# Kernel tuning notes

Measured on AMD Instinct MI355X. Metric: run time of the kernel, lower is better.

Reference implementation:

```python
import jax, jax.numpy as jnp
import numpy as np

EPSILON = 1e-4
MAX_ITER = 10


def setup_inputs() -> dict:
    key = jax.random.key(0)
    k1, k2, k3 = jax.random.split(key, 3)
    B, N, M = 64, 1024, 1024
    s = jax.random.uniform(k1, (B, N, M), dtype=jnp.float32)
    nrows = jax.random.randint(k2, (B,), 0, N, dtype=jnp.int32)
    ncols = jax.random.randint(k3, (B,), 0, M, dtype=jnp.int32)
    return {"s": s, "nrows": nrows, "ncols": ncols}


def reference(s, nrows, ncols):
    # s: [B, N, M]; nrows/ncols: [B] valid row/col counts per sample.
    B, N, M = s.shape
    row_mask = jnp.arange(N, dtype=nrows.dtype)[None, :] < nrows[:, None]  # [B, N]
    col_mask = jnp.arange(M, dtype=ncols.dtype)[None, :] < ncols[:, None]  # [B, M]
    mask = row_mask[:, :, None] & col_mask[:, None, :]  # [B, N, M]

    s = s + EPSILON
    for i in range(MAX_ITER):
        # i even -> column normalization (sum over dim 1); i odd -> row normalization (sum over dim 2)
        axis = 2 if i % 2 == 1 else 1
        ssum = jnp.sum(s, axis=axis, keepdims=True)
        tmp = jnp.where(mask, 1.0 / ssum, jnp.zeros((), dtype=s.dtype))
        s = s * tmp
    return s
```

## Files before the change

kernel.cpp:

```cpp
#include <hip/hip_runtime.h>

#define EPS 1e-4f

constexpr int Bn = 64;
constexpr int Nn = 1024;
constexpr int Mn = 1024;
constexpr int NSPLIT = 16;
constexpr int CHUNK  = Nn / NSPLIT;
constexpr int SLOTS  = 2 * NSPLIT;

__device__ __forceinline__ unsigned pk2(float a, float b) {
    unsigned ua = __float_as_uint(a); ua = (ua + 0x7fffu + ((ua >> 16) & 1u)) >> 16;
    unsigned ub = __float_as_uint(b); ub = (ub + 0x7fffu + ((ub >> 16) & 1u)) >> 16;
    return ua | (ub << 16);
}
__device__ __forceinline__ float lo16(unsigned v) { return __uint_as_float(v << 16); }
__device__ __forceinline__ float hi16(unsigned v) { return __uint_as_float(v & 0xffff0000u); }

__global__ __launch_bounds__(256) void fuse0_kernel(
        const float* __restrict__ s, unsigned short* __restrict__ sc,
        float* __restrict__ p) {
    const int b = blockIdx.x, sp = blockIdx.y;
    const int t = threadIdx.x, half = t >> 7, tc = t & 127;
    float acc[8];
    #pragma unroll
    for (int k = 0; k < 8; ++k) acc[k] = 0.f;
    for (int j = 0; j < CHUNK; j += 2) {
        const int n = sp * CHUNK + j + half;
        const size_t roff = ((size_t)b * Nn + n) * Mn;
        const float4* src = reinterpret_cast<const float4*>(s + roff) + 2 * tc;
        float4 v0 = src[0], v1 = src[1];
        v0.x += EPS; v0.y += EPS; v0.z += EPS; v0.w += EPS;
        v1.x += EPS; v1.y += EPS; v1.z += EPS; v1.w += EPS;
        acc[0] += v0.x; acc[1] += v0.y; acc[2] += v0.z; acc[3] += v0.w;
        acc[4] += v1.x; acc[5] += v1.y; acc[6] += v1.z; acc[7] += v1.w;
        uint4 w = { pk2(v0.x, v0.y), pk2(v0.z, v0.w),
                    pk2(v1.x, v1.y), pk2(v1.z, v1.w) };
        reinterpret_cast<uint4*>(sc + roff)[tc] = w;
    }
    float* pp = p + ((size_t)(b * SLOTS + sp * 2 + half)) * Mn + tc * 8;
    float4 o0 = {acc[0], acc[1], acc[2], acc[3]};
    float4 o1 = {acc[4], acc[5], acc[6], acc[7]};
    *reinterpret_cast<float4*>(pp)     = o0;
    *reinterpret_cast<float4*>(pp + 4) = o1;
}

__global__ __launch_bounds__(256) void colred_kernel(
        const unsigned short* __restrict__ sc, const float* __restrict__ r,
        float* __restrict__ p) {
    const int b = blockIdx.x, sp = blockIdx.y;
    const int t = threadIdx.x, half = t >> 7, tc = t & 127;
    const float* rb = r + (size_t)b * Nn;
    float acc[8];
    #pragma unroll
    for (int k = 0; k < 8; ++k) acc[k] = 0.f;
    #pragma unroll 4
    for (int j = 0; j < CHUNK; j += 2) {
        const int n = sp * CHUNK + j + half;
        uint4 a = reinterpret_cast<const uint4*>(sc + ((size_t)b * Nn + n) * Mn)[tc];
        const float rn = rb[n];
        acc[0] += lo16(a.x) * rn; acc[1] += hi16(a.x) * rn;
        acc[2] += lo16(a.y) * rn; acc[3] += hi16(a.y) * rn;
        acc[4] += lo16(a.z) * rn; acc[5] += hi16(a.z) * rn;
        acc[6] += lo16(a.w) * rn; acc[7] += hi16(a.w) * rn;
    }
    float* pp = p + ((size_t)(b * SLOTS + sp * 2 + half)) * Mn + tc * 8;
    float4 o0 = {acc[0], acc[1], acc[2], acc[3]};
    float4 o1 = {acc[4], acc[5], acc[6], acc[7]};
    *reinterpret_cast<float4*>(pp)     = o0;
    *reinterpret_cast<float4*>(pp + 4) = o1;
}

__global__ __launch_bounds__(256) void col_final_kernel(
        const float* __restrict__ p, const int* __restrict__ ncols,
        float* __restrict__ c) {
    const int b = blockIdx.x;
    const int m0 = threadIdx.x << 2;
    float sx = 0.f, sy = 0.f, sz = 0.f, sw = 0.f;
    #pragma unroll
    for (int k = 0; k < SLOTS; ++k) {
        float4 v = *reinterpret_cast<const float4*>(
            p + ((size_t)(b * SLOTS + k)) * Mn + m0);
        sx += v.x; sy += v.y; sz += v.z; sw += v.w;
    }
    const int nc = ncols[b];
    float4 o;
    o.x = (m0 + 0 < nc && sx > 0.f) ? 1.f / sx : 0.f;
    o.y = (m0 + 1 < nc && sy > 0.f) ? 1.f / sy : 0.f;
    o.z = (m0 + 2 < nc && sz > 0.f) ? 1.f / sz : 0.f;
    o.w = (m0 + 3 < nc && sw > 0.f) ? 1.f / sw : 0.f;
    *reinterpret_cast<float4*>(c + (size_t)b * Mn + m0) = o;
}

__global__ __launch_bounds__(256) void rowred_kernel(
        const unsigned short* __restrict__ sc, const float* __restrict__ c,
        const int* __restrict__ nrows, float* __restrict__ r) {
    const int b = blockIdx.x;
    const int t = threadIdx.x, w = t >> 6, l = t & 63;
    const int n0 = blockIdx.y * 32 + w * 8;
    const float4* cb = reinterpret_cast<const float4*>(c + (size_t)b * Mn);
    const float4 c0 = cb[2 * l], c1 = cb[2 * l + 1];
    const float4 c2 = cb[128 + 2 * l], c3 = cb[128 + 2 * l + 1];
    const int nr = nrows[b];
    for (int j = 0; j < 8; ++j) {
        const int n = n0 + j;
        const uint4* row = reinterpret_cast<const uint4*>(sc + ((size_t)b * Nn + n) * Mn);
        uint4 a = row[l], d = row[64 + l];
        float part =
            lo16(a.x) * c0.x + hi16(a.x) * c0.y + lo16(a.y) * c0.z + hi16(a.y) * c0.w +
            lo16(a.z) * c1.x + hi16(a.z) * c1.y + lo16(a.w) * c1.z + hi16(a.w) * c1.w +
            lo16(d.x) * c2.x + hi16(d.x) * c2.y + lo16(d.y) * c2.z + hi16(d.y) * c2.w +
            lo16(d.z) * c3.x + hi16(d.z) * c3.y + lo16(d.w) * c3.z + hi16(d.w) * c3.w;
        #pragma unroll
        for (int off = 1; off < 64; off <<= 1) part += __shfl_xor(part, off, 64);
        if (l == 0) r[(size_t)b * Nn + n] = (n < nr && part > 0.f) ? 1.f / part : 0.f;
    }
}

__global__ __launch_bounds__(256) void final_kernel(
        const float* __restrict__ s, const float* __restrict__ c,
        const int* __restrict__ nrows, float* __restrict__ out) {
    const int b = blockIdx.x;
    const int t = threadIdx.x, w = t >> 6, l = t & 63;
    const int n0 = blockIdx.y * 32 + w * 8;
    const float4* cb = reinterpret_cast<const float4*>(c + (size_t)b * Mn);
    float4 cc[4];
    #pragma unroll
    for (int k = 0; k < 4; ++k) cc[k] = cb[64 * k + l];
    const int nr = nrows[b];
    for (int j = 0; j < 8; ++j) {
        const int n = n0 + j;
        const size_t roff = ((size_t)b * Nn + n) * Mn;
        const float4* row = reinterpret_cast<const float4*>(s + roff);
        float4 a[4];
        float part = 0.f;
        #pragma unroll
        for (int k = 0; k < 4; ++k) {
            a[k] = row[64 * k + l];
            a[k].x += EPS; a[k].y += EPS; a[k].z += EPS; a[k].w += EPS;
            part += a[k].x * cc[k].x + a[k].y * cc[k].y
                  + a[k].z * cc[k].z + a[k].w * cc[k].w;
        }
        #pragma unroll
        for (int off = 1; off < 64; off <<= 1) part += __shfl_xor(part, off, 64);
        const float rv = (n < nr && part > 0.f) ? 1.f / part : 0.f;
        float4* orow = reinterpret_cast<float4*>(out + roff);
        #pragma unroll
        for (int k = 0; k < 4; ++k) {
            float4 o;
            o.x = a[k].x * cc[k].x * rv;
            o.y = a[k].y * cc[k].y * rv;
            o.z = a[k].z * cc[k].z * rv;
            o.w = a[k].w * cc[k].w * rv;
            orow[64 * k + l] = o;
        }
    }
}

extern "C" void kernel_launch(void* const* d_in, const int* in_sizes, int n_in,
                              void* d_out, int out_size, void* d_ws, size_t ws_size,
                              hipStream_t stream) {
    const float* s     = (const float*)d_in[0];
    const int*   nrows = (const int*)d_in[1];
    const int*   ncols = (const int*)d_in[2];
    float* out = (float*)d_out;

    unsigned short* sc = (unsigned short*)d_ws;
    float* p = (float*)(sc + (size_t)Bn * Nn * Mn);
    float* c = p + (size_t)Bn * SLOTS * Mn;
    float* r = c + (size_t)Bn * Mn;

    fuse0_kernel<<<dim3(Bn, NSPLIT), 256, 0, stream>>>(s, sc, p);
    col_final_kernel<<<Bn, 256, 0, stream>>>(p, ncols, c);
    for (int it = 0; it < 4; ++it) {
        rowred_kernel<<<dim3(Bn, Nn / 32), 256, 0, stream>>>(sc, c, nrows, r);
        colred_kernel<<<dim3(Bn, NSPLIT), 256, 0, stream>>>(sc, r, p);
        col_final_kernel<<<Bn, 256, 0, stream>>>(p, ncols, c);
    }
    final_kernel<<<dim3(Bn, Nn / 32), 256, 0, stream>>>(s, c, nrows, out);
}
```

Before: 738.5 us.

## Fuse row and column reductions into one pass over the bf16 matrix

The separate row-reduction and column-reduction kernels are merged into one. Each wave computes a row's reciprocal sum and, while the row data is still in registers, accumulates that row's contribution to per-column partial sums. This halves the reads of the bf16 copy per Sinkhorn iteration pair and drops one launch per iteration. The cost is more partial-sum slots (64 instead of 32) for the column finalize step to reduce, and higher register use for the 16 accumulators.

Measured after the change: 716.4 us. 1.03x faster.

```diff
diff --git a/kernel.cpp b/kernel.cpp
--- a/kernel.cpp
+++ b/kernel.cpp
@@ -7,7 +7,8 @@
 constexpr int Mn = 1024;
 constexpr int NSPLIT = 16;
 constexpr int CHUNK  = Nn / NSPLIT;
-constexpr int SLOTS  = 2 * NSPLIT;
+constexpr int SLOT0  = 2 * NSPLIT;
+constexpr int SLOT1  = 64;
 
 __device__ __forceinline__ unsigned pk2(float a, float b) {
     unsigned ua = __float_as_uint(a); ua = (ua + 0x7fffu + ((ua >> 16) & 1u)) >> 16;
@@ -38,33 +39,7 @@
                     pk2(v1.x, v1.y), pk2(v1.z, v1.w) };
         reinterpret_cast<uint4*>(sc + roff)[tc] = w;
     }
-    float* pp = p + ((size_t)(b * SLOTS + sp * 2 + half)) * Mn + tc * 8;
-    float4 o0 = {acc[0], acc[1], acc[2], acc[3]};
-    float4 o1 = {acc[4], acc[5], acc[6], acc[7]};
-    *reinterpret_cast<float4*>(pp)     = o0;
-    *reinterpret_cast<float4*>(pp + 4) = o1;
-}
-
-__global__ __launch_bounds__(256) void colred_kernel(
-        const unsigned short* __restrict__ sc, const float* __restrict__ r,
-        float* __restrict__ p) {
-    const int b = blockIdx.x, sp = blockIdx.y;
-    const int t = threadIdx.x, half = t >> 7, tc = t & 127;
-    const float* rb = r + (size_t)b * Nn;
-    float acc[8];
-    #pragma unroll
-    for (int k = 0; k < 8; ++k) acc[k] = 0.f;
-    #pragma unroll 4
-    for (int j = 0; j < CHUNK; j += 2) {
-        const int n = sp * CHUNK + j + half;
-        uint4 a = reinterpret_cast<const uint4*>(sc + ((size_t)b * Nn + n) * Mn)[tc];
-        const float rn = rb[n];
-        acc[0] += lo16(a.x) * rn; acc[1] += hi16(a.x) * rn;
-        acc[2] += lo16(a.y) * rn; acc[3] += hi16(a.y) * rn;
-        acc[4] += lo16(a.z) * rn; acc[5] += hi16(a.z) * rn;
-        acc[6] += lo16(a.w) * rn; acc[7] += hi16(a.w) * rn;
-    }
-    float* pp = p + ((size_t)(b * SLOTS + sp * 2 + half)) * Mn + tc * 8;
+    float* pp = p + ((size_t)(b * SLOT1 + sp * 2 + half)) * Mn + tc * 8;
     float4 o0 = {acc[0], acc[1], acc[2], acc[3]};
     float4 o1 = {acc[4], acc[5], acc[6], acc[7]};
     *reinterpret_cast<float4*>(pp)     = o0;
@@ -73,14 +48,13 @@
 
 __global__ __launch_bounds__(256) void col_final_kernel(
         const float* __restrict__ p, const int* __restrict__ ncols,
-        float* __restrict__ c) {
+        float* __restrict__ c, int slots) {
     const int b = blockIdx.x;
     const int m0 = threadIdx.x << 2;
     float sx = 0.f, sy = 0.f, sz = 0.f, sw = 0.f;
-    #pragma unroll
-    for (int k = 0; k < SLOTS; ++k) {
+    for (int k = 0; k < slots; ++k) {
         float4 v = *reinterpret_cast<const float4*>(
-            p + ((size_t)(b * SLOTS + k)) * Mn + m0);
+            p + ((size_t)(b * SLOT1 + k)) * Mn + m0);
         sx += v.x; sy += v.y; sz += v.z; sw += v.w;
     }
     const int nc = ncols[b];
@@ -92,29 +66,45 @@
     *reinterpret_cast<float4*>(c + (size_t)b * Mn + m0) = o;
 }
 
-__global__ __launch_bounds__(256) void rowred_kernel(
+__global__ __launch_bounds__(256) void rowcol_kernel(
         const unsigned short* __restrict__ sc, const float* __restrict__ c,
-        const int* __restrict__ nrows, float* __restrict__ r) {
+        const int* __restrict__ nrows, float* __restrict__ p) {
     const int b = blockIdx.x;
     const int t = threadIdx.x, w = t >> 6, l = t & 63;
-    const int n0 = blockIdx.y * 32 + w * 8;
+    const int n0 = blockIdx.y * 64 + w * 16;
     const float4* cb = reinterpret_cast<const float4*>(c + (size_t)b * Mn);
     const float4 c0 = cb[2 * l], c1 = cb[2 * l + 1];
     const float4 c2 = cb[128 + 2 * l], c3 = cb[128 + 2 * l + 1];
     const int nr = nrows[b];
-    for (int j = 0; j < 8; ++j) {
+    float acc[16];
+    #pragma unroll
+    for (int k = 0; k < 16; ++k) acc[k] = 0.f;
+    for (int j = 0; j < 16; ++j) {
         const int n = n0 + j;
         const uint4* row = reinterpret_cast<const uint4*>(sc + ((size_t)b * Nn + n) * Mn);
         uint4 a = row[l], d = row[64 + l];
-        float part =
-            lo16(a.x) * c0.x + hi16(a.x) * c0.y + lo16(a.y) * c0.z + hi16(a.y) * c0.w +
-            lo16(a.z) * c1.x + hi16(a.z) * c1.y + lo16(a.w) * c1.z + hi16(a.w) * c1.w +
-            lo16(d.x) * c2.x + hi16(d.x) * c2.y + lo16(d.y) * c2.z + hi16(d.y) * c2.w +
-            lo16(d.z) * c3.x + hi16(d.z) * c3.y + lo16(d.w) * c3.z + hi16(d.w) * c3.w;
+        const float v0 = lo16(a.x), v1 = hi16(a.x), v2 = lo16(a.y), v3 = hi16(a.y);
+        const float v4 = lo16(a.z), v5 = hi16(a.z), v6 = lo16(a.w), v7 = hi16(a.w);
+        const float v8 = lo16(d.x), v9 = hi16(d.x), v10 = lo16(d.y), v11 = hi16(d.y);
+        const float v12 = lo16(d.z), v13 = hi16(d.z), v14 = lo16(d.w), v15 = hi16(d.w);
+        float part = v0 * c0.x + v1 * c0.y + v2 * c0.z + v3 * c0.w
+                   + v4 * c1.x + v5 * c1.y + v6 * c1.z + v7 * c1.w
+                   + v8 * c2.x + v9 * c2.y + v10 * c2.z + v11 * c2.w
+                   + v12 * c3.x + v13 * c3.y + v14 * c3.z + v15 * c3.w;
         #pragma unroll
         for (int off = 1; off < 64; off <<= 1) part += __shfl_xor(part, off, 64);
-        if (l == 0) r[(size_t)b * Nn + n] = (n < nr && part > 0.f) ? 1.f / part : 0.f;
+        const float rv = (n < nr && part > 0.f) ? 1.f / part : 0.f;
+        acc[0]  += v0 * rv;  acc[1]  += v1 * rv;  acc[2]  += v2 * rv;  acc[3]  += v3 * rv;
+        acc[4]  += v4 * rv;  acc[5]  += v5 * rv;  acc[6]  += v6 * rv;  acc[7]  += v7 * rv;
+        acc[8]  += v8 * rv;  acc[9]  += v9 * rv;  acc[10] += v10 * rv; acc[11] += v11 * rv;
+        acc[12] += v12 * rv; acc[13] += v13 * rv; acc[14] += v14 * rv; acc[15] += v15 * rv;
     }
+    float* pp = p + ((size_t)(b * SLOT1) + blockIdx.y * 4 + w) * Mn;
+    float4 o;
+    o = {acc[0], acc[1], acc[2], acc[3]};     *reinterpret_cast<float4*>(pp + 8 * l)           = o;
+    o = {acc[4], acc[5], acc[6], acc[7]};     *reinterpret_cast<float4*>(pp + 8 * l + 4)       = o;
+    o = {acc[8], acc[9], acc[10], acc[11]};   *reinterpret_cast<float4*>(pp + 512 + 8 * l)     = o;
+    o = {acc[12], acc[13], acc[14], acc[15]}; *reinterpret_cast<float4*>(pp + 512 + 8 * l + 4) = o;
 }
 
 __global__ __launch_bounds__(256) void final_kernel(
@@ -167,15 +157,13 @@
 
     unsigned short* sc = (unsigned short*)d_ws;
     float* p = (float*)(sc + (size_t)Bn * Nn * Mn);
-    float* c = p + (size_t)Bn * SLOTS * Mn;
-    float* r = c + (size_t)Bn * Mn;
+    float* c = p + (size_t)Bn * SLOT1 * Mn;
 
     fuse0_kernel<<<dim3(Bn, NSPLIT), 256, 0, stream>>>(s, sc, p);
-    col_final_kernel<<<Bn, 256, 0, stream>>>(p, ncols, c);
+    col_final_kernel<<<Bn, 256, 0, stream>>>(p, ncols, c, SLOT0);
     for (int it = 0; it < 4; ++it) {
-        rowred_kernel<<<dim3(Bn, Nn / 32), 256, 0, stream>>>(sc, c, nrows, r);
-        colred_kernel<<<dim3(Bn, NSPLIT), 256, 0, stream>>>(sc, r, p);
-        col_final_kernel<<<Bn, 256, 0, stream>>>(p, ncols, c);
+        rowcol_kernel<<<dim3(Bn, Nn / 64), 256, 0, stream>>>(sc, c, nrows, p);
+        col_final_kernel<<<Bn, 256, 0, stream>>>(p, ncols, c, SLOT1);
     }
     final_kernel<<<dim3(Bn, Nn / 32), 256, 0, stream>>>(s, c, nrows, out);
 }
```
